# Kernel tuning notes

Measured on AMD Instinct MI355X. Metric: run time of the kernel, lower is better.

The kernel has to match this reference:

```python
import jax, jax.numpy as jnp
import numpy as np

N_NODES = 50000


def _relgraphconv(x, W, Wloop, b, src, dst, etypes, n_nodes):
    # DGL RelGraphConv (regularizer=None, self_loop=True, norm=None):
    # out[i] = sum over incoming edges (j->i, rel r) of W_r @ x[j]  +  W_loop @ x[i]  +  b
    # low-mem form: transform all nodes per relation, then gather per edge.
    h_rel = jnp.einsum('ni,rio->rno', x, W)          # [R, N, out]
    msg = h_rel[etypes, src]                          # [E, out]
    agg = jax.ops.segment_sum(msg, dst, num_segments=n_nodes)  # [N, out]
    return agg + x @ Wloop + b


def setup_inputs() -> dict:
    key = jax.random.key(0)
    ks = jax.random.split(key, 12)
    N, E, n_state = N_NODES, 800000, 128
    inp = {
        'x': jax.random.normal(ks[0], (N, n_state), dtype=jnp.float32),
        'src': jax.random.randint(ks[1], (E,), 0, N, dtype=jnp.int32),
        'dst': jax.random.randint(ks[2], (E,), 0, N, dtype=jnp.int32),
        'etypes': jax.random.randint(ks[3], (E,), 0, 2, dtype=jnp.int32),
        'cell_size': jax.random.randint(ks[4], (N,), 0, 8, dtype=jnp.int32),
        'max_size': jax.random.randint(ks[5], (N,), 0, 8, dtype=jnp.int32),
        'W1': jax.random.normal(ks[6], (2, n_state, 64), dtype=jnp.float32) * 0.05,
        'loop1': jax.random.normal(ks[7], (n_state, 64), dtype=jnp.float32) * 0.05,
        'b1': jnp.zeros((64,), dtype=jnp.float32),
        'W2': jax.random.normal(ks[8], (2, 64, 64), dtype=jnp.float32) * 0.05,
        'loop2': jax.random.normal(ks[9], (64, 64), dtype=jnp.float32) * 0.05,
        'b2': jnp.zeros((64,), dtype=jnp.float32),
        'W3': jax.random.normal(ks[10], (2, 64, 2), dtype=jnp.float32) * 0.05,
        'loop3': jax.random.normal(ks[11], (64, 2), dtype=jnp.float32) * 0.05,
        'b3': jnp.zeros((2,), dtype=jnp.float32),
    }
    return inp


def reference(x, src, dst, etypes, cell_size, max_size,
              W1, loop1, b1, W2, loop2, b2, W3, loop3, b3):
    N = x.shape[0]
    h = jax.nn.relu(_relgraphconv(x, W1, loop1, b1, src, dst, etypes, N))
    h = jax.nn.relu(_relgraphconv(h, W2, loop2, b2, src, dst, etypes, N))
    h = _relgraphconv(h, W3, loop3, b3, src, dst, etypes, N)   # [N, 2]
    # action mask: col 0 = cannot upsize, col 1 = cannot downsize
    upper = cell_size >= (max_size - 1)
    lower = cell_size == 0
    mask = jnp.stack([upper, lower], axis=1)                   # [N, 2] bool
    return jnp.where(mask, h.min() - 1.0, h)
```

## Files before the change

### kernel.cpp

```cpp
#include <hip/hip_runtime.h>


#define STRIDE 64
#define BINCAP 2560

typedef unsigned short ushortT;
typedef __attribute__((ext_vector_type(8))) short short8;
typedef __attribute__((ext_vector_type(4))) float f32x4;

__device__ inline ushortT f2bf(float f) {
    union { float f; unsigned u; } v; v.f = f;
    unsigned r = v.u + 0x7FFFu + ((v.u >> 16) & 1u);
    return (ushortT)(r >> 16);
}
__device__ inline float bf2f(ushortT h) {
    union { unsigned u; float f; } v; v.u = ((unsigned)h) << 16;
    return v.f;
}

__device__ inline void atomicMinF(float* addr, float v) {
    if (v >= 0.f) atomicMin((int*)addr, __float_as_int(v));
    else          atomicMax((unsigned int*)addr, __float_as_uint(v));
}

__global__ __launch_bounds__(256) void pack_phaseA_kernel(
    const float* __restrict__ W1, const float* __restrict__ loop1,
    const float* __restrict__ W2, const float* __restrict__ loop2,
    ushortT* __restrict__ BP1, ushortT* __restrict__ BP2,
    float* __restrict__ minval,
    const int* __restrict__ src, const int* __restrict__ dst,
    const int* __restrict__ et, int* __restrict__ bincnt, int2* __restrict__ binbuf,
    int N, int E, int NBINS) {
    __shared__ int hist[512];
    __shared__ int gbase[512];
    __shared__ ushortT rnk[4096];
    const int t = (int)threadIdx.x;

    if ((int)blockIdx.x < 18) {
        int g = (int)blockIdx.x * 256 + t;
        if (g == 0) *(int*)minval = 0x7f7f7f7f;
        if (g < 3072) {
            int l = g & 63, ks = (g >> 6) & 3, ct = g >> 8;
            int c = ct * 16 + (l & 15);
            int mat = c >> 6, cc = c & 63;
            int kbase = ks * 32 + (l >> 4) * 8;
            ushortT* dstp = BP1 + (size_t)g * 8;
#pragma unroll
            for (int j = 0; j < 8; ++j) {
                int k = kbase + j;
                float v = (mat < 2) ? W1[((size_t)mat * 128 + k) * 64 + cc]
                                    : loop1[(size_t)k * 64 + cc];
                dstp[j] = f2bf(v);
            }
        } else {
            int s = g - 3072;
            int l = s & 63;
            int ks = (s >> 6) % 6;
            int ct = s / 384;
            int c = ct * 16 + (l & 15);
            int kbase = ks * 32 + (l >> 4) * 8;
            ushortT* dstp = BP2 + (size_t)s * 8;
#pragma unroll
            for (int j = 0; j < 8; ++j) {
                int k = kbase + j;
                float v = (k < 128) ? W2[(size_t)k * 64 + c]
                                    : loop2[(size_t)(k - 128) * 64 + c];
                dstp[j] = f2bf(v);
            }
        }
        return;
    }
    for (int i = t; i < NBINS; i += 256) hist[i] = 0;
    __syncthreads();
    const int base = ((int)blockIdx.x - 18) * 4096;
#pragma unroll
    for (int i = 0; i < 16; ++i) {
        int e = base + t + i * 256;
        if (e < E) {
            int bb = dst[e] >> 7;
            rnk[t + i * 256] = (ushortT)atomicAdd(&hist[bb], 1);
        }
    }
    __syncthreads();
    for (int i = t; i < NBINS; i += 256) {
        int h = hist[i];
        gbase[i] = h ? atomicAdd(&bincnt[i], h) : 0;
    }
    __syncthreads();
#pragma unroll
    for (int i = 0; i < 16; ++i) {
        int e = base + t + i * 256;
        if (e < E) {
            int dd = dst[e];
            int bb = dd >> 7;
            int v = et[e] * N + src[e];
            int pos = gbase[bb] + (int)rnk[t + i * 256];
            if (pos < BINCAP)
                binbuf[(size_t)bb * BINCAP + pos] = make_int2(dd, v);
        }
    }
}

__global__ __launch_bounds__(256) void gemm1_phaseB_kernel(
    const float* __restrict__ x, const ushortT* __restrict__ BP1,
    const float* __restrict__ b1,
    ushortT* __restrict__ hrelb, ushortT* __restrict__ H1b,
    const int* __restrict__ bincnt, const int2* __restrict__ binbuf,
    int* __restrict__ cnt, int* __restrict__ eidx,
    int N, int NBINS) {
    __shared__ int lcnt[128];
    const int t = (int)threadIdx.x;

    if ((int)blockIdx.x < NBINS) {
        const int b = (int)blockIdx.x;
        if (t < 128) lcnt[t] = 0;
        __syncthreads();
        const int cb = min(bincnt[b], BINCAP);
        const int2* buf = binbuf + (size_t)b * BINCAP;
        for (int i = t; i < cb; i += 256) {
            int2 rec = buf[i];
            int r = atomicAdd(&lcnt[rec.x & 127], 1);
            if (r < STRIDE) eidx[(size_t)rec.x * STRIDE + r] = rec.y;
        }
        __syncthreads();
        int node = b * 128 + t;
        if (t < 128 && node < N) cnt[node] = min(lcnt[t], STRIDE);
        return;
    }
    const int w = t >> 6, lane = t & 63;
    const int rowbase = (((int)blockIdx.x - NBINS) * 4 + w) * 16;
    const int m = lane & 15, quad = lane >> 4;
    const int nclamp = min(rowbase + m, N - 1);

    short8 a[4];
    const float* xp = x + (size_t)nclamp * 128 + quad * 8;
#pragma unroll
    for (int ks = 0; ks < 4; ++ks) {
        float4 g0 = *(const float4*)(xp + ks * 32);
        float4 g1 = *(const float4*)(xp + ks * 32 + 4);
        a[ks][0] = (short)f2bf(g0.x); a[ks][1] = (short)f2bf(g0.y);
        a[ks][2] = (short)f2bf(g0.z); a[ks][3] = (short)f2bf(g0.w);
        a[ks][4] = (short)f2bf(g1.x); a[ks][5] = (short)f2bf(g1.y);
        a[ks][6] = (short)f2bf(g1.z); a[ks][7] = (short)f2bf(g1.w);
    }

    f32x4 acc[12];
#pragma unroll
    for (int ct = 0; ct < 12; ++ct) acc[ct] = (f32x4){0.f, 0.f, 0.f, 0.f};

#pragma unroll
    for (int ks = 0; ks < 4; ++ks) {
#pragma unroll
        for (int ct = 0; ct < 12; ++ct) {
            short8 b = *(const short8*)&BP1[((size_t)(ct * 4 + ks) * 64 + lane) * 8];
            acc[ct] = __builtin_amdgcn_mfma_f32_16x16x32_bf16(a[ks], b, acc[ct], 0, 0, 0);
        }
    }

    const int node0 = rowbase + quad * 4;
#pragma unroll
    for (int ct = 0; ct < 12; ++ct) {
        int c = ct * 16 + m;
        int mat = c >> 6, cc = c & 63;
        float bias = (mat == 2) ? b1[cc] : 0.f;
#pragma unroll
        for (int j = 0; j < 4; ++j) {
            int n = node0 + j;
            if (n < N) {
                float v = acc[ct][j] + bias;
                if (mat < 2) hrelb[((size_t)mat * N + n) * 64 + cc] = f2bf(v);
                else         H1b[(size_t)n * 64 + cc] = f2bf(v);
            }
        }
    }
}

__device__ __forceinline__ float gather_accum(
    const ushortT* __restrict__ hb, int my, int deg, int lane, float acc) {
    for (int j = 0; j < deg; j += 16) {
        float v[16];
#pragma unroll
        for (int q = 0; q < 16; ++q) {
            int jj = j + q;
            int sel = (jj < deg) ? jj : 0;
            int id = __shfl(my, sel, 64);
            float wgt = (jj < deg) ? 1.f : 0.f;
            v[q] = wgt * bf2f(hb[(size_t)id * 64 + lane]);
        }
        float s0 = (v[0] + v[1]) + (v[2] + v[3]);
        float s1 = (v[4] + v[5]) + (v[6] + v[7]);
        float s2 = (v[8] + v[9]) + (v[10] + v[11]);
        float s3 = (v[12] + v[13]) + (v[14] + v[15]);
        acc += (s0 + s1) + (s2 + s3);
    }
    return acc;
}

__global__ void agg1_kernel(const ushortT* __restrict__ hrelb, const int* __restrict__ eidx,
                            const int* __restrict__ cnt, ushortT* __restrict__ H1b, int N) {
    int node = (int)blockIdx.x * 4 + ((int)threadIdx.x >> 6);
    if (node >= N) return;
    int lane = (int)threadIdx.x & 63;
    int deg = cnt[node];
    int my = (lane < deg) ? eidx[(size_t)node * STRIDE + lane] : 0;
    float acc = bf2f(H1b[(size_t)node * 64 + lane]);
    acc = gather_accum(hrelb, my, deg, lane, acc);
    H1b[(size_t)node * 64 + lane] = f2bf(fmaxf(acc, 0.f));
}

__global__ void agg2_kernel(const ushortT* __restrict__ H1b, const int* __restrict__ eidx,
                            const int* __restrict__ cnt, ushortT* __restrict__ Sb, int N) {
    int node = (int)blockIdx.x * 4 + ((int)threadIdx.x >> 6);
    if (node >= N) return;
    int lane = (int)threadIdx.x & 63;
    int deg = cnt[node];
    int my = (lane < deg) ? eidx[(size_t)node * STRIDE + lane] : 0;
    float a0 = 0.f, a1 = 0.f;
    for (int j = 0; j < deg; j += 16) {
        float v[16], w0[16], w1[16];
#pragma unroll
        for (int q = 0; q < 16; ++q) {
            int jj = j + q;
            int sel = (jj < deg) ? jj : 0;
            int id = __shfl(my, sel, 64);
            int rel = (id >= N) ? 1 : 0;
            int row = id - rel * N;
            float live = (jj < deg) ? 1.f : 0.f;
            w0[q] = rel ? 0.f : live;
            w1[q] = rel ? live : 0.f;
            v[q] = bf2f(H1b[(size_t)row * 64 + lane]);
        }
#pragma unroll
        for (int q = 0; q < 16; ++q) {
            a0 += w0[q] * v[q];
            a1 += w1[q] * v[q];
        }
    }
    Sb[(size_t)node * 64 + lane] = f2bf(a0);
    Sb[((size_t)N + node) * 64 + lane] = f2bf(a1);
}

__global__ __launch_bounds__(256) void gemm23_kernel(
    const ushortT* __restrict__ Sb, const ushortT* __restrict__ H1b,
    const ushortT* __restrict__ BP2, const float* __restrict__ b2,
    const float* __restrict__ W3, const float* __restrict__ loop3,
    const float* __restrict__ b3,
    float* __restrict__ hrel3, float* __restrict__ H3, int N) {
    const int w = (int)threadIdx.x >> 6, lane = (int)threadIdx.x & 63;
    const int rowbase = ((int)blockIdx.x * 4 + w) * 16;
    const int m = lane & 15, quad = lane >> 4;
    const int nclamp = min(rowbase + m, N - 1);

    f32x4 acc[4];
#pragma unroll
    for (int ct = 0; ct < 4; ++ct) acc[ct] = (f32x4){0.f, 0.f, 0.f, 0.f};

#pragma unroll
    for (int ks = 0; ks < 6; ++ks) {
        const ushortT* base =
            (ks < 2) ? (Sb + (size_t)nclamp * 64)
          : (ks < 4) ? (Sb + ((size_t)N + nclamp) * 64)
                     : (H1b + (size_t)nclamp * 64);
        short8 a = *(const short8*)(base + (ks & 1) * 32 + quad * 8);
#pragma unroll
        for (int ct = 0; ct < 4; ++ct) {
            short8 b = *(const short8*)&BP2[((size_t)(ct * 6 + ks) * 64 + lane) * 8];
            acc[ct] = __builtin_amdgcn_mfma_f32_16x16x32_bf16(a, b, acc[ct], 0, 0, 0);
        }
    }

    float h2[4][4];
#pragma unroll
    for (int ct = 0; ct < 4; ++ct) {
        float bias = b2[ct * 16 + m];
#pragma unroll
        for (int j = 0; j < 4; ++j) h2[ct][j] = fmaxf(acc[ct][j] + bias, 0.f);
    }

    float w3v[4][6];
#pragma unroll
    for (int ct = 0; ct < 4; ++ct) {
        int k = ct * 16 + m;
        w3v[ct][0] = W3[k * 2 + 0];
        w3v[ct][1] = W3[k * 2 + 1];
        w3v[ct][2] = W3[(64 + k) * 2 + 0];
        w3v[ct][3] = W3[(64 + k) * 2 + 1];
        w3v[ct][4] = loop3[k * 2 + 0];
        w3v[ct][5] = loop3[k * 2 + 1];
    }
    float p[4][6];
#pragma unroll
    for (int j = 0; j < 4; ++j)
#pragma unroll
        for (int c = 0; c < 6; ++c) p[j][c] = 0.f;
#pragma unroll
    for (int j = 0; j < 4; ++j)
#pragma unroll
        for (int ct = 0; ct < 4; ++ct)
#pragma unroll
            for (int c = 0; c < 6; ++c) p[j][c] += h2[ct][j] * w3v[ct][c];

#pragma unroll
    for (int mask = 1; mask <= 8; mask <<= 1) {
#pragma unroll
        for (int j = 0; j < 4; ++j)
#pragma unroll
            for (int c = 0; c < 6; ++c) p[j][c] += __shfl_xor(p[j][c], mask, 64);
    }

    if (m == 0) {
#pragma unroll
        for (int j = 0; j < 4; ++j) {
            int n = rowbase + quad * 4 + j;
            if (n < N) {
                hrel3[(size_t)n * 2 + 0] = p[j][0];
                hrel3[(size_t)n * 2 + 1] = p[j][1];
                hrel3[((size_t)N + n) * 2 + 0] = p[j][2];
                hrel3[((size_t)N + n) * 2 + 1] = p[j][3];
                H3[(size_t)n * 2 + 0] = p[j][4] + b3[0];
                H3[(size_t)n * 2 + 1] = p[j][5] + b3[1];
            }
        }
    }
}

__global__ void agg3min_kernel(const float* __restrict__ hrel3, const int* __restrict__ eidx,
                               const int* __restrict__ cnt, float* __restrict__ H3,
                               float* __restrict__ minval, int N) {
    int n = (int)blockIdx.x * 256 + (int)threadIdx.x;
    float v = 3.4e38f;
    if (n < N) {
        float a0 = H3[n * 2 + 0], a1 = H3[n * 2 + 1];
        int deg = cnt[n];
        const int* row = &eidx[(size_t)n * STRIDE];
        for (int j = 0; j < deg; j += 8) {
            float2 q[8];
            float wg[8];
#pragma unroll
            for (int qq = 0; qq < 8; ++qq) {
                int jj = j + qq;
                int sel = (jj < deg) ? jj : 0;
                int idx = row[sel];
                wg[qq] = (jj < deg) ? 1.f : 0.f;
                q[qq] = *(const float2*)&hrel3[(size_t)idx * 2];
            }
#pragma unroll
            for (int qq = 0; qq < 8; ++qq) {
                a0 += wg[qq] * q[qq].x;
                a1 += wg[qq] * q[qq].y;
            }
        }
        H3[n * 2 + 0] = a0;
        H3[n * 2 + 1] = a1;
        v = fminf(a0, a1);
    }
#pragma unroll
    for (int mm = 32; mm >= 1; mm >>= 1) v = fminf(v, __shfl_xor(v, mm, 64));
    __shared__ float s[4];
    if ((threadIdx.x & 63) == 0) s[threadIdx.x >> 6] = v;
    __syncthreads();
    if (threadIdx.x == 0)
        atomicMinF(minval, fminf(fminf(s[0], s[1]), fminf(s[2], s[3])));
}

__global__ void mask_kernel(const float* __restrict__ H3, const float* __restrict__ minval,
                            const int* __restrict__ cs, const int* __restrict__ ms,
                            float* __restrict__ out, int N) {
    int n = (int)blockIdx.x * 256 + (int)threadIdx.x;
    if (n >= N) return;
    float m = minval[0] - 1.0f;
    bool up = cs[n] >= ms[n] - 1;
    bool lo = cs[n] == 0;
    out[n * 2 + 0] = up ? m : H3[n * 2 + 0];
    out[n * 2 + 1] = lo ? m : H3[n * 2 + 1];
}

extern "C" void kernel_launch(void* const* d_in, const int* in_sizes, int n_in,
                              void* d_out, int out_size, void* d_ws, size_t ws_size,
                              hipStream_t stream) {
    const float* x     = (const float*)d_in[0];
    const int* src     = (const int*)d_in[1];
    const int* dst     = (const int*)d_in[2];
    const int* etypes  = (const int*)d_in[3];
    const int* cellsz  = (const int*)d_in[4];
    const int* maxsz   = (const int*)d_in[5];
    const float* W1    = (const float*)d_in[6];
    const float* loop1 = (const float*)d_in[7];
    const float* b1    = (const float*)d_in[8];
    const float* W2    = (const float*)d_in[9];
    const float* loop2 = (const float*)d_in[10];
    const float* b2    = (const float*)d_in[11];
    const float* W3    = (const float*)d_in[12];
    const float* loop3 = (const float*)d_in[13];
    const float* b3    = (const float*)d_in[14];
    float* out = (float*)d_out;

    const int N = in_sizes[0] / 128;
    const int E = in_sizes[1];

    char* p = (char*)d_ws;
    auto alloc = [&](size_t bytes) -> void* {
        void* r = (void*)p;
        p += ((bytes + 255) / 256) * 256;
        return r;
    };
    ushortT* hrelb  = (ushortT*)alloc((size_t)2 * N * 64 * 2);
    ushortT* H1b    = (ushortT*)alloc((size_t)N * 64 * 2);
    ushortT* Sb     = (ushortT*)alloc((size_t)2 * N * 64 * 2);
    float* hrel3    = (float*)alloc((size_t)2 * N * 2 * 4);
    float* H3       = (float*)alloc((size_t)N * 2 * 4);
    int* cnt        = (int*)alloc((size_t)N * 4);
    int* eidx       = (int*)alloc((size_t)N * STRIDE * 4);
    ushortT* BP1    = (ushortT*)alloc((size_t)3072 * 8 * 2);
    ushortT* BP2    = (ushortT*)alloc((size_t)1536 * 8 * 2);
    float* minval   = (float*)alloc(4);

    const int NBINS = (N + 127) >> 7;
    int* bincnt     = (int*)alloc((size_t)NBINS * 4);
    int2* binbuf    = (int2*)alloc((size_t)NBINS * BINCAP * 8);
    (void)ws_size; (void)n_in; (void)out_size;

    const int NB_N   = (N + 255) / 256;
    const int NTILES = (N + 63) / 64;
    const int NB_W   = (N + 3) / 4;
    const int NBA    = (E + 4095) / 4096;

    hipMemsetAsync(bincnt, 0, (size_t)NBINS * 4, stream);

    pack_phaseA_kernel<<<18 + NBA, 256, 0, stream>>>(
        W1, loop1, W2, loop2, BP1, BP2, minval,
        src, dst, etypes, bincnt, binbuf, N, E, NBINS);

    gemm1_phaseB_kernel<<<NBINS + NTILES, 256, 0, stream>>>(
        x, BP1, b1, hrelb, H1b, bincnt, binbuf, cnt, eidx, N, NBINS);

    agg1_kernel<<<NB_W, 256, 0, stream>>>(hrelb, eidx, cnt, H1b, N);

    agg2_kernel<<<NB_W, 256, 0, stream>>>(H1b, eidx, cnt, Sb, N);

    gemm23_kernel<<<NTILES, 256, 0, stream>>>(Sb, H1b, BP2, b2, W3, loop3, b3,
                                              hrel3, H3, N);

    agg3min_kernel<<<NB_N, 256, 0, stream>>>(hrel3, eidx, cnt, H3, minval, N);

    mask_kernel<<<NB_N, 256, 0, stream>>>(H3, minval, cellsz, maxsz, out, N);
}
```

Before: 223.2 us.

## Fuse all stages into one cooperative persistent kernel with grid syncs

Turns the seven-kernel pipeline into a single cooperative mega-kernel whose stages are separated by grid-wide barriers, with blocks striding over tasks. Phase A edge binning is interleaved with the first GEMM in one task loop. A fallback path keeps the multi-kernel launch sequence. The aim is to remove per-kernel launch gaps and drain tails. The cost is grid-sync overhead, occupancy capped by __launch_bounds__(256,4), and one large shared-memory footprint per block that limits how many blocks stay resident.

Result: slower. 713.3 us (+219.5%).

```diff
diff --git a/kernel.cpp b/kernel.cpp
--- a/kernel.cpp
+++ b/kernel.cpp
@@ -1,4 +1,5 @@
 #include <hip/hip_runtime.h>
+#include <hip/hip_cooperative_groups.h>
 
 
 #define STRIDE 64
@@ -7,6 +8,20 @@
 typedef unsigned short ushortT;
 typedef __attribute__((ext_vector_type(8))) short short8;
 typedef __attribute__((ext_vector_type(4))) float f32x4;
+
+struct GP {
+    const float* x; const int* src; const int* dst; const int* et;
+    const int* cellsz; const int* maxsz;
+    const float* W1; const float* loop1; const float* b1;
+    const float* W2; const float* loop2; const float* b2;
+    const float* W3; const float* loop3; const float* b3;
+    float* out;
+    ushortT* hrelb; ushortT* H1b; ushortT* Sb;
+    float* hrel3; float* H3; int* cnt; int* eidx;
+    ushortT* BP1; ushortT* BP2; float* minval;
+    int* bincnt; int2* binbuf;
+    int N, E, NBINS, NBA, NTILES, NB_W, NB_N;
+};
 
 __device__ inline ushortT f2bf(float f) {
     union { float f; unsigned u; } v; v.f = f;
@@ -17,123 +32,86 @@
     union { unsigned u; float f; } v; v.u = ((unsigned)h) << 16;
     return v.f;
 }
-
 __device__ inline void atomicMinF(float* addr, float v) {
     if (v >= 0.f) atomicMin((int*)addr, __float_as_int(v));
     else          atomicMax((unsigned int*)addr, __float_as_uint(v));
 }
 
-__global__ __launch_bounds__(256) void pack_phaseA_kernel(
-    const float* __restrict__ W1, const float* __restrict__ loop1,
-    const float* __restrict__ W2, const float* __restrict__ loop2,
-    ushortT* __restrict__ BP1, ushortT* __restrict__ BP2,
-    float* __restrict__ minval,
-    const int* __restrict__ src, const int* __restrict__ dst,
-    const int* __restrict__ et, int* __restrict__ bincnt, int2* __restrict__ binbuf,
-    int N, int E, int NBINS) {
-    __shared__ int hist[512];
-    __shared__ int gbase[512];
-    __shared__ ushortT rnk[4096];
-    const int t = (int)threadIdx.x;
-
-    if ((int)blockIdx.x < 18) {
-        int g = (int)blockIdx.x * 256 + t;
-        if (g == 0) *(int*)minval = 0x7f7f7f7f;
-        if (g < 3072) {
-            int l = g & 63, ks = (g >> 6) & 3, ct = g >> 8;
-            int c = ct * 16 + (l & 15);
-            int mat = c >> 6, cc = c & 63;
-            int kbase = ks * 32 + (l >> 4) * 8;
-            ushortT* dstp = BP1 + (size_t)g * 8;
-#pragma unroll
-            for (int j = 0; j < 8; ++j) {
-                int k = kbase + j;
-                float v = (mat < 2) ? W1[((size_t)mat * 128 + k) * 64 + cc]
-                                    : loop1[(size_t)k * 64 + cc];
-                dstp[j] = f2bf(v);
-            }
-        } else {
-            int s = g - 3072;
-            int l = s & 63;
-            int ks = (s >> 6) % 6;
-            int ct = s / 384;
-            int c = ct * 16 + (l & 15);
-            int kbase = ks * 32 + (l >> 4) * 8;
-            ushortT* dstp = BP2 + (size_t)s * 8;
-#pragma unroll
-            for (int j = 0; j < 8; ++j) {
-                int k = kbase + j;
-                float v = (k < 128) ? W2[(size_t)k * 64 + c]
-                                    : loop2[(size_t)(k - 128) * 64 + c];
-                dstp[j] = f2bf(v);
-            }
-        }
-        return;
-    }
-    for (int i = t; i < NBINS; i += 256) hist[i] = 0;
+
+__device__ __forceinline__ void dev_pack_init(int g, const GP& p) {
+    if (g == 0) *(int*)p.minval = 0x7f7f7f7f;
+    if (g < 3072) {
+        int l = g & 63, ks = (g >> 6) & 3, ct = g >> 8;
+        int c = ct * 16 + (l & 15);
+        int mat = c >> 6, cc = c & 63;
+        int kbase = ks * 32 + (l >> 4) * 8;
+        ushortT* dstp = p.BP1 + (size_t)g * 8;
+#pragma unroll
+        for (int j = 0; j < 8; ++j) {
+            int k = kbase + j;
+            float v = (mat < 2) ? p.W1[((size_t)mat * 128 + k) * 64 + cc]
+                                : p.loop1[(size_t)k * 64 + cc];
+            dstp[j] = f2bf(v);
+        }
+    } else if (g < 4608) {
+        int s = g - 3072;
+        int l = s & 63;
+        int ks = (s >> 6) % 6;
+        int ct = s / 384;
+        int c = ct * 16 + (l & 15);
+        int kbase = ks * 32 + (l >> 4) * 8;
+        ushortT* dstp = p.BP2 + (size_t)s * 8;
+#pragma unroll
+        for (int j = 0; j < 8; ++j) {
+            int k = kbase + j;
+            float v = (k < 128) ? p.W2[(size_t)k * 64 + c]
+                                : p.loop2[(size_t)(k - 128) * 64 + c];
+            dstp[j] = f2bf(v);
+        }
+    }
+}
+
+__device__ __forceinline__ void dev_phaseA_chunk(
+    int chunk, int t, int* hist, int* gbase, ushortT* rnk, const GP& p) {
+    for (int i = t; i < p.NBINS; i += 256) hist[i] = 0;
     __syncthreads();
-    const int base = ((int)blockIdx.x - 18) * 4096;
+    const int base = chunk * 4096;
 #pragma unroll
     for (int i = 0; i < 16; ++i) {
         int e = base + t + i * 256;
-        if (e < E) {
-            int bb = dst[e] >> 7;
+        if (e < p.E) {
+            int bb = p.dst[e] >> 7;
             rnk[t + i * 256] = (ushortT)atomicAdd(&hist[bb], 1);
         }
     }
     __syncthreads();
-    for (int i = t; i < NBINS; i += 256) {
+    for (int i = t; i < p.NBINS; i += 256) {
         int h = hist[i];
-        gbase[i] = h ? atomicAdd(&bincnt[i], h) : 0;
+        gbase[i] = h ? atomicAdd(&p.bincnt[i], h) : 0;
     }
     __syncthreads();
 #pragma unroll
     for (int i = 0; i < 16; ++i) {
         int e = base + t + i * 256;
-        if (e < E) {
-            int dd = dst[e];
+        if (e < p.E) {
+            int dd = p.dst[e];
             int bb = dd >> 7;
-            int v = et[e] * N + src[e];
+            int v = p.et[e] * p.N + p.src[e];
             int pos = gbase[bb] + (int)rnk[t + i * 256];
             if (pos < BINCAP)
-                binbuf[(size_t)bb * BINCAP + pos] = make_int2(dd, v);
-        }
-    }
-}
-
-__global__ __launch_bounds__(256) void gemm1_phaseB_kernel(
-    const float* __restrict__ x, const ushortT* __restrict__ BP1,
-    const float* __restrict__ b1,
-    ushortT* __restrict__ hrelb, ushortT* __restrict__ H1b,
-    const int* __restrict__ bincnt, const int2* __restrict__ binbuf,
-    int* __restrict__ cnt, int* __restrict__ eidx,
-    int N, int NBINS) {
-    __shared__ int lcnt[128];
-    const int t = (int)threadIdx.x;
-
-    if ((int)blockIdx.x < NBINS) {
-        const int b = (int)blockIdx.x;
-        if (t < 128) lcnt[t] = 0;
-        __syncthreads();
-        const int cb = min(bincnt[b], BINCAP);
-        const int2* buf = binbuf + (size_t)b * BINCAP;
-        for (int i = t; i < cb; i += 256) {
-            int2 rec = buf[i];
-            int r = atomicAdd(&lcnt[rec.x & 127], 1);
-            if (r < STRIDE) eidx[(size_t)rec.x * STRIDE + r] = rec.y;
-        }
-        __syncthreads();
-        int node = b * 128 + t;
-        if (t < 128 && node < N) cnt[node] = min(lcnt[t], STRIDE);
-        return;
-    }
+                p.binbuf[(size_t)bb * BINCAP + pos] = make_int2(dd, v);
+        }
+    }
+}
+
+__device__ __forceinline__ void dev_gemm1_tile(int tile, int t, const GP& p) {
     const int w = t >> 6, lane = t & 63;
-    const int rowbase = (((int)blockIdx.x - NBINS) * 4 + w) * 16;
+    const int rowbase = (tile * 4 + w) * 16;
     const int m = lane & 15, quad = lane >> 4;
-    const int nclamp = min(rowbase + m, N - 1);
+    const int nclamp = min(rowbase + m, p.N - 1);
 
     short8 a[4];
-    const float* xp = x + (size_t)nclamp * 128 + quad * 8;
+    const float* xp = p.x + (size_t)nclamp * 128 + quad * 8;
 #pragma unroll
     for (int ks = 0; ks < 4; ++ks) {
         float4 g0 = *(const float4*)(xp + ks * 32);
@@ -143,36 +121,48 @@
         a[ks][4] = (short)f2bf(g1.x); a[ks][5] = (short)f2bf(g1.y);
         a[ks][6] = (short)f2bf(g1.z); a[ks][7] = (short)f2bf(g1.w);
     }
-
     f32x4 acc[12];
 #pragma unroll
     for (int ct = 0; ct < 12; ++ct) acc[ct] = (f32x4){0.f, 0.f, 0.f, 0.f};
-
 #pragma unroll
     for (int ks = 0; ks < 4; ++ks) {
 #pragma unroll
         for (int ct = 0; ct < 12; ++ct) {
-            short8 b = *(const short8*)&BP1[((size_t)(ct * 4 + ks) * 64 + lane) * 8];
+            short8 b = *(const short8*)&p.BP1[((size_t)(ct * 4 + ks) * 64 + lane) * 8];
             acc[ct] = __builtin_amdgcn_mfma_f32_16x16x32_bf16(a[ks], b, acc[ct], 0, 0, 0);
         }
     }
-
     const int node0 = rowbase + quad * 4;
 #pragma unroll
     for (int ct = 0; ct < 12; ++ct) {
         int c = ct * 16 + m;
         int mat = c >> 6, cc = c & 63;
-        float bias = (mat == 2) ? b1[cc] : 0.f;
+        float bias = (mat == 2) ? p.b1[cc] : 0.f;
 #pragma unroll
         for (int j = 0; j < 4; ++j) {
             int n = node0 + j;
-            if (n < N) {
+            if (n < p.N) {
                 float v = acc[ct][j] + bias;
-                if (mat < 2) hrelb[((size_t)mat * N + n) * 64 + cc] = f2bf(v);
-                else         H1b[(size_t)n * 64 + cc] = f2bf(v);
+                if (mat < 2) p.hrelb[((size_t)mat * p.N + n) * 64 + cc] = f2bf(v);
+                else         p.H1b[(size_t)n * 64 + cc] = f2bf(v);
             }
         }
     }
+}
+
+__device__ __forceinline__ void dev_phaseB_bin(int b, int t, int* lcnt, const GP& p) {
+    if (t < 128) lcnt[t] = 0;
+    __syncthreads();
+    const int cb = min(p.bincnt[b], BINCAP);
+    const int2* buf = p.binbuf + (size_t)b * BINCAP;
+    for (int i = t; i < cb; i += 256) {
+        int2 rec = buf[i];
+        int r = atomicAdd(&lcnt[rec.x & 127], 1);
+        if (r < STRIDE) p.eidx[(size_t)rec.x * STRIDE + r] = rec.y;
+    }
+    __syncthreads();
+    int node = b * 128 + t;
+    if (t < 128 && node < p.N) p.cnt[node] = min(lcnt[t], STRIDE);
 }
 
 __device__ __forceinline__ float gather_accum(
@@ -196,25 +186,23 @@
     return acc;
 }
 
-__global__ void agg1_kernel(const ushortT* __restrict__ hrelb, const int* __restrict__ eidx,
-                            const int* __restrict__ cnt, ushortT* __restrict__ H1b, int N) {
-    int node = (int)blockIdx.x * 4 + ((int)threadIdx.x >> 6);
-    if (node >= N) return;
-    int lane = (int)threadIdx.x & 63;
-    int deg = cnt[node];
-    int my = (lane < deg) ? eidx[(size_t)node * STRIDE + lane] : 0;
-    float acc = bf2f(H1b[(size_t)node * 64 + lane]);
-    acc = gather_accum(hrelb, my, deg, lane, acc);
-    H1b[(size_t)node * 64 + lane] = f2bf(fmaxf(acc, 0.f));
-}
-
-__global__ void agg2_kernel(const ushortT* __restrict__ H1b, const int* __restrict__ eidx,
-                            const int* __restrict__ cnt, ushortT* __restrict__ Sb, int N) {
-    int node = (int)blockIdx.x * 4 + ((int)threadIdx.x >> 6);
-    if (node >= N) return;
-    int lane = (int)threadIdx.x & 63;
-    int deg = cnt[node];
-    int my = (lane < deg) ? eidx[(size_t)node * STRIDE + lane] : 0;
+__device__ __forceinline__ void dev_agg1_group(int blk, int t, const GP& p) {
+    int node = blk * 4 + (t >> 6);
+    if (node >= p.N) return;
+    int lane = t & 63;
+    int deg = p.cnt[node];
+    int my = (lane < deg) ? p.eidx[(size_t)node * STRIDE + lane] : 0;
+    float acc = bf2f(p.H1b[(size_t)node * 64 + lane]);
+    acc = gather_accum(p.hrelb, my, deg, lane, acc);
+    p.H1b[(size_t)node * 64 + lane] = f2bf(fmaxf(acc, 0.f));
+}
+
+__device__ __forceinline__ void dev_agg2_group(int blk, int t, const GP& p) {
+    int node = blk * 4 + (t >> 6);
+    if (node >= p.N) return;
+    int lane = t & 63;
+    int deg = p.cnt[node];
+    int my = (lane < deg) ? p.eidx[(size_t)node * STRIDE + lane] : 0;
     float a0 = 0.f, a1 = 0.f;
     for (int j = 0; j < deg; j += 16) {
         float v[16], w0[16], w1[16];
@@ -223,12 +211,12 @@
             int jj = j + q;
             int sel = (jj < deg) ? jj : 0;
             int id = __shfl(my, sel, 64);
-            int rel = (id >= N) ? 1 : 0;
-            int row = id - rel * N;
+            int rel = (id >= p.N) ? 1 : 0;
+            int row = id - rel * p.N;
             float live = (jj < deg) ? 1.f : 0.f;
             w0[q] = rel ? 0.f : live;
             w1[q] = rel ? live : 0.f;
-            v[q] = bf2f(H1b[(size_t)row * 64 + lane]);
+            v[q] = bf2f(p.H1b[(size_t)row * 64 + lane]);
         }
 #pragma unroll
         for (int q = 0; q < 16; ++q) {
@@ -236,103 +224,91 @@
             a1 += w1[q] * v[q];
         }
     }
-    Sb[(size_t)node * 64 + lane] = f2bf(a0);
-    Sb[((size_t)N + node) * 64 + lane] = f2bf(a1);
-}
-
-__global__ __launch_bounds__(256) void gemm23_kernel(
-    const ushortT* __restrict__ Sb, const ushortT* __restrict__ H1b,
-    const ushortT* __restrict__ BP2, const float* __restrict__ b2,
-    const float* __restrict__ W3, const float* __restrict__ loop3,
-    const float* __restrict__ b3,
-    float* __restrict__ hrel3, float* __restrict__ H3, int N) {
-    const int w = (int)threadIdx.x >> 6, lane = (int)threadIdx.x & 63;
-    const int rowbase = ((int)blockIdx.x * 4 + w) * 16;
+    p.Sb[(size_t)node * 64 + lane] = f2bf(a0);
+    p.Sb[((size_t)p.N + node) * 64 + lane] = f2bf(a1);
+}
+
+__device__ __forceinline__ void dev_gemm23_tile(int tile, int t, const GP& p) {
+    const int w = t >> 6, lane = t & 63;
+    const int rowbase = (tile * 4 + w) * 16;
     const int m = lane & 15, quad = lane >> 4;
-    const int nclamp = min(rowbase + m, N - 1);
+    const int nclamp = min(rowbase + m, p.N - 1);
 
     f32x4 acc[4];
 #pragma unroll
     for (int ct = 0; ct < 4; ++ct) acc[ct] = (f32x4){0.f, 0.f, 0.f, 0.f};
-
 #pragma unroll
     for (int ks = 0; ks < 6; ++ks) {
         const ushortT* base =
-            (ks < 2) ? (Sb + (size_t)nclamp * 64)
-          : (ks < 4) ? (Sb + ((size_t)N + nclamp) * 64)
-                     : (H1b + (size_t)nclamp * 64);
+            (ks < 2) ? (p.Sb + (size_t)nclamp * 64)
+          : (ks < 4) ? (p.Sb + ((size_t)p.N + nclamp) * 64)
+                     : (p.H1b + (size_t)nclamp * 64);
         short8 a = *(const short8*)(base + (ks & 1) * 32 + quad * 8);
 #pragma unroll
         for (int ct = 0; ct < 4; ++ct) {
-            short8 b = *(const short8*)&BP2[((size_t)(ct * 6 + ks) * 64 + lane) * 8];
+            short8 b = *(const short8*)&p.BP2[((size_t)(ct * 6 + ks) * 64 + lane) * 8];
             acc[ct] = __builtin_amdgcn_mfma_f32_16x16x32_bf16(a, b, acc[ct], 0, 0, 0);
         }
     }
-
     float h2[4][4];
 #pragma unroll
     for (int ct = 0; ct < 4; ++ct) {
-        float bias = b2[ct * 16 + m];
+        float bias = p.b2[ct * 16 + m];
 #pragma unroll
         for (int j = 0; j < 4; ++j) h2[ct][j] = fmaxf(acc[ct][j] + bias, 0.f);
     }
-
     float w3v[4][6];
 #pragma unroll
     for (int ct = 0; ct < 4; ++ct) {
         int k = ct * 16 + m;
-        w3v[ct][0] = W3[k * 2 + 0];
-        w3v[ct][1] = W3[k * 2 + 1];
-        w3v[ct][2] = W3[(64 + k) * 2 + 0];
-        w3v[ct][3] = W3[(64 + k) * 2 + 1];
-        w3v[ct][4] = loop3[k * 2 + 0];
-        w3v[ct][5] = loop3[k * 2 + 1];
-    }
-    float p[4][6];
+        w3v[ct][0] = p.W3[k * 2 + 0];
+        w3v[ct][1] = p.W3[k * 2 + 1];
+        w3v[ct][2] = p.W3[(64 + k) * 2 + 0];
+        w3v[ct][3] = p.W3[(64 + k) * 2 + 1];
+        w3v[ct][4] = p.loop3[k * 2 + 0];
+        w3v[ct][5] = p.loop3[k * 2 + 1];
+    }
+    float pr[4][6];
 #pragma unroll
     for (int j = 0; j < 4; ++j)
 #pragma unroll
-        for (int c = 0; c < 6; ++c) p[j][c] = 0.f;
+        for (int c = 0; c < 6; ++c) pr[j][c] = 0.f;
 #pragma unroll
     for (int j = 0; j < 4; ++j)
 #pragma unroll
         for (int ct = 0; ct < 4; ++ct)
 #pragma unroll
-            for (int c = 0; c < 6; ++c) p[j][c] += h2[ct][j] * w3v[ct][c];
-
+            for (int c = 0; c < 6; ++c) pr[j][c] += h2[ct][j] * w3v[ct][c];
 #pragma unroll
     for (int mask = 1; mask <= 8; mask <<= 1) {
 #pragma unroll
         for (int j = 0; j < 4; ++j)
 #pragma unroll
-            for (int c = 0; c < 6; ++c) p[j][c] += __shfl_xor(p[j][c], mask, 64);
-    }
-
+            for (int c = 0; c < 6; ++c) pr[j][c] += __shfl_xor(pr[j][c], mask, 64);
+    }
     if (m == 0) {
 #pragma unroll
         for (int j = 0; j < 4; ++j) {
             int n = rowbase + quad * 4 + j;
-            if (n < N) {
-                hrel3[(size_t)n * 2 + 0] = p[j][0];
-                hrel3[(size_t)n * 2 + 1] = p[j][1];
-                hrel3[((size_t)N + n) * 2 + 0] = p[j][2];
-                hrel3[((size_t)N + n) * 2 + 1] = p[j][3];
-                H3[(size_t)n * 2 + 0] = p[j][4] + b3[0];
-                H3[(size_t)n * 2 + 1] = p[j][5] + b3[1];
+            if (n < p.N) {
+                p.hrel3[(size_t)n * 2 + 0] = pr[j][0];
+                p.hrel3[(size_t)n * 2 + 1] = pr[j][1];
+                p.hrel3[((size_t)p.N + n) * 2 + 0] = pr[j][2];
+                p.hrel3[((size_t)p.N + n) * 2 + 1] = pr[j][3];
+                p.H3[(size_t)n * 2 + 0] = pr[j][4] + p.b3[0];
+                p.H3[(size_t)n * 2 + 1] = pr[j][5] + p.b3[1];
             }
         }
     }
 }
 
-__global__ void agg3min_kernel(const float* __restrict__ hrel3, const int* __restrict__ eidx,
-                               const int* __restrict__ cnt, float* __restrict__ H3,
-                               float* __restrict__ minval, int N) {
-    int n = (int)blockIdx.x * 256 + (int)threadIdx.x;
+__device__ __forceinline__ void dev_agg3min_group(int blk, int t, float* smin, const GP& p) {
+    int n = blk * 256 + t;
     float v = 3.4e38f;
-    if (n < N) {
-        float a0 = H3[n * 2 + 0], a1 = H3[n * 2 + 1];
-        int deg = cnt[n];
-        const int* row = &eidx[(size_t)n * STRIDE];
+    if (n < p.N) {
+        float a0 = p.H3[n * 2 + 0], a1 = p.H3[n * 2 + 1];
+        int deg = p.cnt[n];
+        const int* row = &p.eidx[(size_t)n * STRIDE];
         for (int j = 0; j < deg; j += 8) {
             float2 q[8];
             float wg[8];
@@ -342,7 +318,7 @@
                 int sel = (jj < deg) ? jj : 0;
                 int idx = row[sel];
                 wg[qq] = (jj < deg) ? 1.f : 0.f;
-                q[qq] = *(const float2*)&hrel3[(size_t)idx * 2];
+                q[qq] = *(const float2*)&p.hrel3[(size_t)idx * 2];
             }
 #pragma unroll
             for (int qq = 0; qq < 8; ++qq) {
@@ -350,98 +326,189 @@
                 a1 += wg[qq] * q[qq].y;
             }
         }
-        H3[n * 2 + 0] = a0;
-        H3[n * 2 + 1] = a1;
+        p.H3[n * 2 + 0] = a0;
+        p.H3[n * 2 + 1] = a1;
         v = fminf(a0, a1);
     }
 #pragma unroll
     for (int mm = 32; mm >= 1; mm >>= 1) v = fminf(v, __shfl_xor(v, mm, 64));
-    __shared__ float s[4];
-    if ((threadIdx.x & 63) == 0) s[threadIdx.x >> 6] = v;
+    if ((t & 63) == 0) smin[t >> 6] = v;
     __syncthreads();
-    if (threadIdx.x == 0)
-        atomicMinF(minval, fminf(fminf(s[0], s[1]), fminf(s[2], s[3])));
-}
-
-__global__ void mask_kernel(const float* __restrict__ H3, const float* __restrict__ minval,
-                            const int* __restrict__ cs, const int* __restrict__ ms,
-                            float* __restrict__ out, int N) {
-    int n = (int)blockIdx.x * 256 + (int)threadIdx.x;
-    if (n >= N) return;
-    float m = minval[0] - 1.0f;
-    bool up = cs[n] >= ms[n] - 1;
-    bool lo = cs[n] == 0;
-    out[n * 2 + 0] = up ? m : H3[n * 2 + 0];
-    out[n * 2 + 1] = lo ? m : H3[n * 2 + 1];
-}
+    if (t == 0)
+        atomicMinF(p.minval, fminf(fminf(smin[0], smin[1]), fminf(smin[2], smin[3])));
+}
+
+__device__ __forceinline__ void dev_mask_group(int blk, int t, const GP& p) {
+    int n = blk * 256 + t;
+    if (n >= p.N) return;
+    float m = p.minval[0] - 1.0f;
+    bool up = p.cellsz[n] >= p.maxsz[n] - 1;
+    bool lo = p.cellsz[n] == 0;
+    p.out[n * 2 + 0] = up ? m : p.H3[n * 2 + 0];
+    p.out[n * 2 + 1] = lo ? m : p.H3[n * 2 + 1];
+}
+
+__global__ __launch_bounds__(256, 4) void mega_kernel(GP p) {
+    cooperative_groups::grid_group grid = cooperative_groups::this_grid();
+    __shared__ int hist[512];
+    __shared__ int gbase[512];
+    __shared__ ushortT rnk[4096];
+    __shared__ int lcnt[128];
+    __shared__ float smin[4];
+    const int t = (int)threadIdx.x;
+    const int nb = (int)gridDim.x;
+
+    for (int g = (int)blockIdx.x * 256 + t; g < 4608; g += nb * 256)
+        dev_pack_init(g, p);
+    grid.sync();
+
+    for (int task = (int)blockIdx.x; task < p.NBA + p.NTILES; task += nb) {
+        if (task < p.NBA) dev_phaseA_chunk(task, t, hist, gbase, rnk, p);
+        else              dev_gemm1_tile(task - p.NBA, t, p);
+        __syncthreads();
+    }
+    grid.sync();
+
+    for (int b = (int)blockIdx.x; b < p.NBINS; b += nb) {
+        dev_phaseB_bin(b, t, lcnt, p);
+        __syncthreads();
+    }
+    grid.sync();
+
+    for (int blk = (int)blockIdx.x; blk < p.NB_W; blk += nb)
+        dev_agg1_group(blk, t, p);
+    grid.sync();
+
+    for (int blk = (int)blockIdx.x; blk < p.NB_W; blk += nb)
+        dev_agg2_group(blk, t, p);
+    grid.sync();
+
+    for (int tile = (int)blockIdx.x; tile < p.NTILES; tile += nb)
+        dev_gemm23_tile(tile, t, p);
+    grid.sync();
+
+    for (int blk = (int)blockIdx.x; blk < p.NB_N; blk += nb) {
+        dev_agg3min_group(blk, t, smin, p);
+        __syncthreads();
+    }
+    grid.sync();
+
+    for (int blk = (int)blockIdx.x; blk < p.NB_N; blk += nb)
+        dev_mask_group(blk, t, p);
+}
+
+__global__ __launch_bounds__(256) void fb_pack_phaseA(GP p) {
+    __shared__ int hist[512];
+    __shared__ int gbase[512];
+    __shared__ ushortT rnk[4096];
+    const int t = (int)threadIdx.x;
+    if ((int)blockIdx.x < 18) {
+        dev_pack_init((int)blockIdx.x * 256 + t, p);
+        return;
+    }
+    dev_phaseA_chunk((int)blockIdx.x - 18, t, hist, gbase, rnk, p);
+}
+__global__ __launch_bounds__(256) void fb_gemm1_phaseB(GP p) {
+    __shared__ int lcnt[128];
+    const int t = (int)threadIdx.x;
+    if ((int)blockIdx.x < p.NBINS) {
+        dev_phaseB_bin((int)blockIdx.x, t, lcnt, p);
+        return;
+    }
+    dev_gemm1_tile((int)blockIdx.x - p.NBINS, t, p);
+}
+__global__ void fb_agg1(GP p)   { dev_agg1_group((int)blockIdx.x, (int)threadIdx.x, p); }
+__global__ void fb_agg2(GP p)   { dev_agg2_group((int)blockIdx.x, (int)threadIdx.x, p); }
+__global__ __launch_bounds__(256) void fb_gemm23(GP p) {
+    dev_gemm23_tile((int)blockIdx.x, (int)threadIdx.x, p);
+}
+__global__ void fb_agg3min(GP p) {
+    __shared__ float smin[4];
+    dev_agg3min_group((int)blockIdx.x, (int)threadIdx.x, smin, p);
+}
+__global__ void fb_mask(GP p)   { dev_mask_group((int)blockIdx.x, (int)threadIdx.x, p); }
 
 extern "C" void kernel_launch(void* const* d_in, const int* in_sizes, int n_in,
                               void* d_out, int out_size, void* d_ws, size_t ws_size,
                               hipStream_t stream) {
-    const float* x     = (const float*)d_in[0];
-    const int* src     = (const int*)d_in[1];
-    const int* dst     = (const int*)d_in[2];
-    const int* etypes  = (const int*)d_in[3];
-    const int* cellsz  = (const int*)d_in[4];
-    const int* maxsz   = (const int*)d_in[5];
-    const float* W1    = (const float*)d_in[6];
-    const float* loop1 = (const float*)d_in[7];
-    const float* b1    = (const float*)d_in[8];
-    const float* W2    = (const float*)d_in[9];
-    const float* loop2 = (const float*)d_in[10];
-    const float* b2    = (const float*)d_in[11];
-    const float* W3    = (const float*)d_in[12];
-    const float* loop3 = (const float*)d_in[13];
-    const float* b3    = (const float*)d_in[14];
-    float* out = (float*)d_out;
-
     const int N = in_sizes[0] / 128;
     const int E = in_sizes[1];
 
-    char* p = (char*)d_ws;
+    char* pw = (char*)d_ws;
     auto alloc = [&](size_t bytes) -> void* {
-        void* r = (void*)p;
-        p += ((bytes + 255) / 256) * 256;
+        void* r = (void*)pw;
+        pw += ((bytes + 255) / 256) * 256;
         return r;
     };
-    ushortT* hrelb  = (ushortT*)alloc((size_t)2 * N * 64 * 2);
-    ushortT* H1b    = (ushortT*)alloc((size_t)N * 64 * 2);
-    ushortT* Sb     = (ushortT*)alloc((size_t)2 * N * 64 * 2);
-    float* hrel3    = (float*)alloc((size_t)2 * N * 2 * 4);
-    float* H3       = (float*)alloc((size_t)N * 2 * 4);
-    int* cnt        = (int*)alloc((size_t)N * 4);
-    int* eidx       = (int*)alloc((size_t)N * STRIDE * 4);
-    ushortT* BP1    = (ushortT*)alloc((size_t)3072 * 8 * 2);
-    ushortT* BP2    = (ushortT*)alloc((size_t)1536 * 8 * 2);
-    float* minval   = (float*)alloc(4);
+    GP p;
+    p.x      = (const float*)d_in[0];
+    p.src    = (const int*)d_in[1];
+    p.dst    = (const int*)d_in[2];
+    p.et     = (const int*)d_in[3];
+    p.cellsz = (const int*)d_in[4];
+    p.maxsz  = (const int*)d_in[5];
+    p.W1     = (const float*)d_in[6];
+    p.loop1  = (const float*)d_in[7];
+    p.b1     = (const float*)d_in[8];
+    p.W2     = (const float*)d_in[9];
+    p.loop2  = (const float*)d_in[10];
+    p.b2     = (const float*)d_in[11];
+    p.W3     = (const float*)d_in[12];
+    p.loop3  = (const float*)d_in[13];
+    p.b3     = (const float*)d_in[14];
+    p.out    = (float*)d_out;
+
+    p.hrelb  = (ushortT*)alloc((size_t)2 * N * 64 * 2);
+    p.H1b    = (ushortT*)alloc((size_t)N * 64 * 2);
+    p.Sb     = (ushortT*)alloc((size_t)2 * N * 64 * 2);
+    p.hrel3  = (float*)alloc((size_t)2 * N * 2 * 4);
+    p.H3     = (float*)alloc((size_t)N * 2 * 4);
+    p.cnt    = (int*)alloc((size_t)N * 4);
+    p.eidx   = (int*)alloc((size_t)N * STRIDE * 4);
+    p.BP1    = (ushortT*)alloc((size_t)3072 * 8 * 2);
+    p.BP2    = (ushortT*)alloc((size_t)1536 * 8 * 2);
+    p.minval = (float*)alloc(4);
 
     const int NBINS = (N + 127) >> 7;
-    int* bincnt     = (int*)alloc((size_t)NBINS * 4);
-    int2* binbuf    = (int2*)alloc((size_t)NBINS * BINCAP * 8);
+    p.bincnt = (int*)alloc((size_t)NBINS * 4);
+    p.binbuf = (int2*)alloc((size_t)NBINS * BINCAP * 8);
+
+    p.N = N; p.E = E; p.NBINS = NBINS;
+    p.NBA    = (E + 4095) / 4096;
+    p.NTILES = (N + 63) / 64;
+    p.NB_W   = (N + 3) / 4;
+    p.NB_N   = (N + 255) / 256;
     (void)ws_size; (void)n_in; (void)out_size;
 
-    const int NB_N   = (N + 255) / 256;
-    const int NTILES = (N + 63) / 64;
-    const int NB_W   = (N + 3) / 4;
-    const int NBA    = (E + 4095) / 4096;
-
-    hipMemsetAsync(bincnt, 0, (size_t)NBINS * 4, stream);
-
-    pack_phaseA_kernel<<<18 + NBA, 256, 0, stream>>>(
-        W1, loop1, W2, loop2, BP1, BP2, minval,
-        src, dst, etypes, bincnt, binbuf, N, E, NBINS);
-
-    gemm1_phaseB_kernel<<<NBINS + NTILES, 256, 0, stream>>>(
-        x, BP1, b1, hrelb, H1b, bincnt, binbuf, cnt, eidx, N, NBINS);
-
-    agg1_kernel<<<NB_W, 256, 0, stream>>>(hrelb, eidx, cnt, H1b, N);
-
-    agg2_kernel<<<NB_W, 256, 0, stream>>>(H1b, eidx, cnt, Sb, N);
-
-    gemm23_kernel<<<NTILES, 256, 0, stream>>>(Sb, H1b, BP2, b2, W3, loop3, b3,
-                                              hrel3, H3, N);
-
-    agg3min_kernel<<<NB_N, 256, 0, stream>>>(hrel3, eidx, cnt, H3, minval, N);
-
-    mask_kernel<<<NB_N, 256, 0, stream>>>(H3, minval, cellsz, maxsz, out, N);
-}
+    hipMemsetAsync(p.bincnt, 0, (size_t)NBINS * 4, stream);
+
+    int dev = 0;
+    hipGetDevice(&dev);
+    hipDeviceProp_t prop;
+    bool coop = (hipGetDeviceProperties(&prop, dev) == hipSuccess) &&
+                (prop.cooperativeLaunch != 0);
+    int grid = 0;
+    if (coop) {
+        int maxBlk = 0;
+        if (hipOccupancyMaxActiveBlocksPerMultiprocessor(
+                &maxBlk, (const void*)mega_kernel, 256, 0) == hipSuccess &&
+            maxBlk > 0) {
+            grid = maxBlk * prop.multiProcessorCount;
+            if (grid > 2048) grid = 2048;
+        }
+    }
+    if (grid >= 256) {
+        void* args[] = { (void*)&p };
+        hipError_t e = hipLaunchCooperativeKernel(
+            (const void*)mega_kernel, dim3(grid), dim3(256), args, 0, stream);
+        if (e == hipSuccess) return;
+    }
+
+    fb_pack_phaseA<<<18 + p.NBA, 256, 0, stream>>>(p);
+    fb_gemm1_phaseB<<<p.NBINS + p.NTILES, 256, 0, stream>>>(p);
+    fb_agg1<<<p.NB_W, 256, 0, stream>>>(p);
+    fb_agg2<<<p.NB_W, 256, 0, stream>>>(p);
+    fb_gemm23<<<p.NTILES, 256, 0, stream>>>(p);
+    fb_agg3min<<<p.NB_N, 256, 0, stream>>>(p);
+    fb_mask<<<p.NB_N, 256, 0, stream>>>(p);
+}
```
